# Kernel optimization log

Hardware: AMD Instinct MI355X
Metric: run time of the kernel (lower is better)

The kernel has to match this reference:

```python
import jax, jax.numpy as jnp
import numpy as np

B, N, E, H = 2, 4096, 768, 8
D = E // H
SCALING = float(D ** 0.5)


def setup_inputs() -> dict:
    key = jax.random.key(0)
    ks = jax.random.split(key, 9)
    s = 1.0 / np.sqrt(E)
    return {
        "x": jax.random.normal(ks[0], (B, N, E), dtype=jnp.float32),
        "Wq": jax.random.normal(ks[1], (E, E), dtype=jnp.float32) * s,
        "bq": jax.random.normal(ks[2], (E,), dtype=jnp.float32) * s,
        "Wk": jax.random.normal(ks[3], (E, E), dtype=jnp.float32) * s,
        "bk": jax.random.normal(ks[4], (E,), dtype=jnp.float32) * s,
        "Wv": jax.random.normal(ks[5], (E, E), dtype=jnp.float32) * s,
        "bv": jax.random.normal(ks[6], (E,), dtype=jnp.float32) * s,
        "Wo": jax.random.normal(ks[7], (E, E), dtype=jnp.float32) * s,
        "bo": jax.random.normal(ks[8], (E,), dtype=jnp.float32) * s,
    }


def reference(x, Wq, bq, Wk, bk, Wv, bv, Wo, bo):
    b, n, e = x.shape
    # projections, split heads: [b, n, e] -> [b, h, n, d]
    def split_heads(y):
        return y.reshape(b, n, H, D).transpose(0, 2, 1, 3)
    q = split_heads(x @ Wq + bq)
    k = split_heads(x @ Wk + bk)
    v = split_heads(x @ Wv + bv)
    # full quadratic attention matrix, as in the original einsum
    energy = jnp.einsum("bhqd,bhkd->bhqk", q, k)  # [b, h, n, n]
    # NOTE: original divides by scaling AFTER softmax (not before)
    att = jax.nn.softmax(energy, axis=-1) / SCALING
    out = jnp.einsum("bhqk,bhkd->bhqd", att, v)  # [b, h, n, d]
    out = out.transpose(0, 2, 1, 3).reshape(b, n, e)  # merge heads
    return out @ Wo + bo
```

## Files before the change

### kernel.cpp

```cpp
#include <hip/hip_runtime.h>
#include <hip/hip_bf16.h>


typedef unsigned short u16;
typedef unsigned long long u64;
typedef __attribute__((ext_vector_type(4))) float f32x4;
typedef __attribute__((ext_vector_type(8))) _Float16 h16x8;
typedef __attribute__((ext_vector_type(2))) __fp16 fp16x2;
typedef __attribute__((ext_vector_type(8))) u16 u16x8;

#define DEVI static __device__ __forceinline__

#define GLD16(gp, lp)                                                          \
  __builtin_amdgcn_global_load_lds(                                            \
      (const __attribute__((address_space(1))) void*)(gp),                     \
      (__attribute__((address_space(3))) void*)(lp), 16, 0, 0)
#define VM_WAIT6() asm volatile("s_waitcnt vmcnt(6)" ::: "memory")
#define VM_WAIT4() asm volatile("s_waitcnt vmcnt(4)" ::: "memory")
#define VM_WAIT0() asm volatile("s_waitcnt vmcnt(0)" ::: "memory")
#define BARRAW()   asm volatile("s_barrier" ::: "memory")

DEVI u16 f2h(float f) {
  _Float16 h = (_Float16)f;
  return __builtin_bit_cast(u16, h);
}

DEVI unsigned pkrtz(float a, float b) {
  fp16x2 h = __builtin_amdgcn_cvt_pkrtz(a, b);
  return __builtin_bit_cast(unsigned, h);
}

DEVI float exp2fast(float x) {
#if __has_builtin(__builtin_amdgcn_exp2f)
  return __builtin_amdgcn_exp2f(x);
#else
  return __expf(x * 0.6931471805599453f);
#endif
}

DEVI f32x4 mfma16(u16x8 a, u16x8 b, f32x4 c) {
  return __builtin_amdgcn_mfma_f32_16x16x32_f16(
      __builtin_bit_cast(h16x8, a), __builtin_bit_cast(h16x8, b), c, 0, 0, 0);
}

__global__ void k_cast(const float* __restrict__ x, u16* __restrict__ xh, int n8) {
  int i = blockIdx.x * blockDim.x + threadIdx.x;
  if (i >= n8) return;
  const f32x4* p = (const f32x4*)x + (size_t)i * 2;
  f32x4 a = p[0], b = p[1];
  u16x8 o;
  #pragma unroll
  for (int u = 0; u < 4; ++u) { o[u] = f2h(a[u]); o[4 + u] = f2h(b[u]); }
  *((u16x8*)xh + i) = o;
}

__global__ void k_wt(const float* __restrict__ Wq, const float* __restrict__ Wk,
                     const float* __restrict__ Wv, const float* __restrict__ Wo,
                     u16* __restrict__ wT) {
  __shared__ __align__(16) float T[64 * 68];
  int bid = blockIdx.x;
  int mat = bid / 144, tt = bid % 144;
  int tr = tt / 12, tc = tt % 12;
  const float* W = (mat == 0) ? Wq : (mat == 1) ? Wk : (mat == 2) ? Wv : Wo;
  int k0 = tr * 64, n0 = tc * 64;
  int t = threadIdx.x;
  #pragma unroll
  for (int ii = 0; ii < 4; ++ii) {
    int i = t + 256 * ii, r = i >> 4, c4 = i & 15;
    f32x4 v = *(const f32x4*)(W + (size_t)(k0 + r) * 768 + n0 + c4 * 4);
    *(f32x4*)(&T[r * 68 + c4 * 4]) = v;
  }
  __syncthreads();
  #pragma unroll
  for (int ii = 0; ii < 2; ++ii) {
    int i = t + 256 * ii, nn = i & 63, kc8 = i >> 6;
    u16x8 o;
    #pragma unroll
    for (int u = 0; u < 8; ++u) o[u] = f2h(T[(kc8 * 8 + u) * 68 + nn]);
    *(u16x8*)(wT + (size_t)mat * 589824 + (size_t)(n0 + nn) * 768 + k0 + kc8 * 8) = o;
  }
}

__global__ void k_vt(const u16* __restrict__ V, u16* __restrict__ Vt) {
  __shared__ __align__(16) u16 L[64 * 104];
  int bid = blockIdx.x, bh = bid >> 6, nb = bid & 63;
  int n0 = nb * 64, t = threadIdx.x;
  const u16* src = V + ((size_t)bh * 4096 + n0) * 96;
  #pragma unroll
  for (int ii = 0; ii < 3; ++ii) {
    int i = t + 256 * ii, r = i / 12, c8 = i % 12;
    *(u16x8*)(&L[r * 104 + c8 * 8]) = *(const u16x8*)(src + (size_t)i * 8);
  }
  __syncthreads();
  #pragma unroll
  for (int jj = 0; jj < 3; ++jj) {
    int d = (t & 31) + 32 * jj, c8 = t >> 5;
    u16x8 o;
    #pragma unroll
    for (int u = 0; u < 8; ++u) o[u] = L[(c8 * 8 + u) * 104 + d];
    *(u16x8*)(Vt + ((size_t)bh * 96 + d) * 4096 + n0 + c8 * 8) = o;
  }
}

template <int MODE>
__global__ __launch_bounds__(256) void k_gemm(
    const u16* __restrict__ A, const u16* __restrict__ BT,
    const float* __restrict__ bias0, const float* __restrict__ bias1,
    const float* __restrict__ bias2,
    u16* __restrict__ Qb, u16* __restrict__ Kb, u16* __restrict__ Vb,
    float* __restrict__ Out) {
  __shared__ __align__(16) u16 sg[16384];
  const int m0 = blockIdx.x * 128, n0 = blockIdx.y * 128;
  const int t = threadIdx.x, w = t >> 6, lane = t & 63;
  const int g = lane >> 4, c = lane & 15;
  const int wr = w >> 1, wc = w & 1;

  const u16* ap[2]; const u16* bp[2]; int lo[2];
  #pragma unroll
  for (int ii = 0; ii < 2; ++ii) {
    int i = t + 256 * ii;
    ap[ii] = A + (size_t)(m0 + (i >> 2)) * 768 + (i & 3) * 8;
    bp[ii] = BT + (size_t)(n0 + (i >> 2)) * 768 + (i & 3) * 8;
    lo[ii] = (i & ~63) * 8;
  }
  auto STAGE = [&](int buf) {
    #pragma unroll
    for (int ii = 0; ii < 2; ++ii) {
      GLD16(ap[ii], &sg[buf * 4096 + lo[ii]]);
      GLD16(bp[ii], &sg[8192 + buf * 4096 + lo[ii]]);
      ap[ii] += 32; bp[ii] += 32;
    }
  };

  f32x4 acc[4][4] = {};
  STAGE(0);
  #pragma unroll 1
  for (int kk = 0; kk < 24; ++kk) {
    const int cur = kk & 1;
    if (kk < 23) { STAGE(cur ^ 1); VM_WAIT4(); } else { VM_WAIT0(); }
    BARRAW();
    u16x8 af[4], bf[4];
    #pragma unroll
    for (int mt = 0; mt < 4; ++mt)
      af[mt] = *(u16x8*)(&sg[cur * 4096 + (wr * 64 + mt * 16 + c) * 32 + g * 8]);
    #pragma unroll
    for (int nt = 0; nt < 4; ++nt)
      bf[nt] = *(u16x8*)(&sg[8192 + cur * 4096 + (wc * 64 + nt * 16 + c) * 32 + g * 8]);
    #pragma unroll
    for (int mt = 0; mt < 4; ++mt)
      #pragma unroll
      for (int nt = 0; nt < 4; ++nt)
        acc[mt][nt] = mfma16(af[mt], bf[nt], acc[mt][nt]);
    BARRAW();
  }

  if (MODE == 0) {
    const int mat = n0 / 768;
    const float* bias = (mat == 0) ? bias0 : (mat == 1) ? bias1 : bias2;
    u16* dst = (mat == 0) ? Qb : (mat == 1) ? Kb : Vb;
    const float qsc = (mat == 0) ? 1.44269504f : 1.0f;
    const int nbase = n0 - mat * 768;
    #pragma unroll
    for (int mt = 0; mt < 4; ++mt)
      #pragma unroll
      for (int nt = 0; nt < 4; ++nt) {
        int ncol = nbase + wc * 64 + nt * 16 + c;
        int h = ncol / 96, d = ncol % 96;
        float bi = bias[ncol];
        #pragma unroll
        for (int r = 0; r < 4; ++r) {
          int mrow = m0 + wr * 64 + mt * 16 + g * 4 + r;
          int b = mrow >> 12, ntok = mrow & 4095;
          dst[((size_t)((b * 8 + h) * 4096 + ntok)) * 96 + d] =
              f2h((acc[mt][nt][r] + bi) * qsc);
        }
      }
  } else {
    #pragma unroll
    for (int mt = 0; mt < 4; ++mt)
      #pragma unroll
      for (int nt = 0; nt < 4; ++nt) {
        int ncol = n0 + wc * 64 + nt * 16 + c;
        float bi = bias0[ncol];
        #pragma unroll
        for (int r = 0; r < 4; ++r) {
          int mrow = m0 + wr * 64 + mt * 16 + g * 4 + r;
          Out[(size_t)mrow * 768 + ncol] = acc[mt][nt][r] + bi;
        }
      }
  }
}

__global__ __launch_bounds__(256) void k_attn(
    const u16* __restrict__ Q, const u16* __restrict__ K,
    const u16* __restrict__ Vt, u16* __restrict__ attn) {
  __shared__ __align__(16) u16 smem[34816];

  const int bid = blockIdx.x;
  const int bh = bid >> 5, qb = bid & 31;
  const int t = threadIdx.x, w = t >> 6, lane = t & 63;
  const int g = lane >> 4, c = lane & 15;
  const int q0 = qb * 128;

  u16x8 qf[3][2];
  #pragma unroll
  for (int qc = 0; qc < 2; ++qc) {
    const size_t qoff = ((size_t)bh * 4096 + q0 + w * 32 + qc * 16 + c) * 96;
    #pragma unroll
    for (int kc = 0; kc < 3; ++kc)
      qf[kc][qc] = *(const u16x8*)(Q + qoff + kc * 32 + g * 8);
  }
  VM_WAIT0();

  const u16* Kbb = K + (size_t)bh * 4096 * 96;
  const u16* Vtb = Vt + (size_t)bh * 96 * 4096;
  const u16* ks[3]; const u16* vs[3]; int ko[3], vo[3];
  #pragma unroll
  for (int ii = 0; ii < 3; ++ii) {
    int ci = t + 256 * ii;
    ks[ii] = Kbb + ci * 8;
    int d = ci >> 3, c8 = ci & 7;
    vs[ii] = Vtb + (size_t)d * 4096 + ((c8 ^ (d & 7)) * 8);
    ko[ii] = (ci & ~63) * 8;
    vo[ii] = 12288 + (ci & ~63) * 8;
  }
  auto STAGE = [&](int buf) {
    #pragma unroll
    for (int ii = 0; ii < 3; ++ii) {
      GLD16(ks[ii], &smem[buf * 6144 + ko[ii]]);
      GLD16(vs[ii], &smem[buf * 6144 + vo[ii]]);
      ks[ii] += 6144;
      vs[ii] += 64;
    }
  };

  f32x4 acc_o[6][2] = {};
  float m[2] = {-1e30f, -1e30f}, s[2] = {0.f, 0.f};
  u16* Pw = &smem[24576 + w * 2560];

  STAGE(0);
  #pragma unroll 1
  for (int tt = 0; tt < 64; ++tt) {
    const int cur = tt & 1;
    if (tt < 63) { STAGE(cur ^ 1); VM_WAIT6(); } else { VM_WAIT0(); }
    BARRAW();
    const u16* Kl = &smem[cur * 6144];
    const u16* Vl = &smem[12288 + cur * 6144];

    f32x4 et[4][2] = {};
    #pragma unroll
    for (int kc = 0; kc < 3; ++kc)
      #pragma unroll
      for (int mt = 0; mt < 4; ++mt) {
        u16x8 kf = *(const u16x8*)(&Kl[(mt * 16 + c) * 96 + kc * 32 + g * 8]);
        et[mt][0] = mfma16(kf, qf[kc][0], et[mt][0]);
        et[mt][1] = mfma16(kf, qf[kc][1], et[mt][1]);
      }

    #pragma unroll
    for (int qc = 0; qc < 2; ++qc) {
      float t0 = fmaxf(fmaxf(et[0][qc][0], et[0][qc][1]),
                       fmaxf(et[0][qc][2], et[0][qc][3]));
      float t1 = fmaxf(fmaxf(et[1][qc][0], et[1][qc][1]),
                       fmaxf(et[1][qc][2], et[1][qc][3]));
      float t2 = fmaxf(fmaxf(et[2][qc][0], et[2][qc][1]),
                       fmaxf(et[2][qc][2], et[2][qc][3]));
      float t3 = fmaxf(fmaxf(et[3][qc][0], et[3][qc][1]),
                       fmaxf(et[3][qc][2], et[3][qc][3]));
      float tmax = fmaxf(fmaxf(t0, t1), fmaxf(t2, t3));
      tmax = fmaxf(tmax, __shfl_xor(tmax, 16));
      tmax = fmaxf(tmax, __shfl_xor(tmax, 32));
      bool upd = tmax > m[qc] + 12.0f;
      float mnew = upd ? tmax : m[qc];
      if (__any(upd)) {
        float sc = exp2fast(m[qc] - mnew);
        s[qc] *= sc;
        #pragma unroll
        for (int dt = 0; dt < 6; ++dt)
          #pragma unroll
          for (int r = 0; r < 4; ++r) acc_o[dt][qc][r] *= sc;
      }
      m[qc] = mnew;
      float psum = 0.f;
      #pragma unroll
      for (int mt = 0; mt < 4; ++mt)
        #pragma unroll
        for (int r = 0; r < 4; ++r) {
          float p = exp2fast(et[mt][qc][r] - mnew);
          et[mt][qc][r] = p; psum += p;
        }
      psum += __shfl_xor(psum, 16);
      psum += __shfl_xor(psum, 32);
      s[qc] += psum;

      u16* P = Pw + qc * 1280;
      #pragma unroll
      for (int mt = 0; mt < 4; ++mt) {
        unsigned p0 = pkrtz(et[mt][qc][0], et[mt][qc][1]);
        unsigned p1 = pkrtz(et[mt][qc][2], et[mt][qc][3]);
        *(u64*)(&P[c * 80 + mt * 16 + g * 4]) = (u64)p0 | ((u64)p1 << 32);
      }
    }
    u16x8 pf[2][2];
    #pragma unroll
    for (int qc = 0; qc < 2; ++qc)
      #pragma unroll
      for (int kb = 0; kb < 2; ++kb)
        pf[qc][kb] = *(u16x8*)(&Pw[qc * 1280 + c * 80 + kb * 32 + g * 8]);
    #pragma unroll
    for (int dt = 0; dt < 6; ++dt)
      #pragma unroll
      for (int kb = 0; kb < 2; ++kb) {
        u16x8 vf = *(u16x8*)(&Vl[(dt * 16 + c) * 64 + (((kb * 4 + g) ^ (c & 7)) * 8)]);
        acc_o[dt][0] = mfma16(vf, pf[0][kb], acc_o[dt][0]);
        acc_o[dt][1] = mfma16(vf, pf[1][kb], acc_o[dt][1]);
      }
    BARRAW();
  }

  __syncthreads();
  u16* O = smem;
  #pragma unroll
  for (int qc = 0; qc < 2; ++qc) {
    const float inv = 1.0f / (s[qc] * 9.797958971132712f);
    #pragma unroll
    for (int dt = 0; dt < 6; ++dt)
      #pragma unroll
      for (int rp = 0; rp < 2; ++rp) {
        unsigned pk = (unsigned)f2h(acc_o[dt][qc][2 * rp] * inv) |
                      ((unsigned)f2h(acc_o[dt][qc][2 * rp + 1] * inv) << 16);
        *(unsigned*)(&O[(w * 32 + qc * 16 + c) * 96 + dt * 16 + g * 4 + 2 * rp]) = pk;
      }
  }
  __syncthreads();
  const int b = bh >> 3, h = bh & 7;
  #pragma unroll
  for (int ii = 0; ii < 6; ++ii) {
    int i = t + 256 * ii, r = i / 12, c8 = i % 12;
    u16x8 v = *(u16x8*)(&O[r * 96 + c8 * 8]);
    *(u16x8*)(attn + ((size_t)(b * 4096 + q0 + r)) * 768 + h * 96 + c8 * 8) = v;
  }
}

extern "C" void kernel_launch(void* const* d_in, const int* in_sizes, int n_in,
                              void* d_out, int out_size, void* d_ws, size_t ws_size,
                              hipStream_t stream) {
  const float* x  = (const float*)d_in[0];
  const float* Wq = (const float*)d_in[1];
  const float* bq = (const float*)d_in[2];
  const float* Wk = (const float*)d_in[3];
  const float* bk = (const float*)d_in[4];
  const float* Wv = (const float*)d_in[5];
  const float* bv = (const float*)d_in[6];
  const float* Wo = (const float*)d_in[7];
  const float* bo = (const float*)d_in[8];
  float* out = (float*)d_out;

  char* ws = (char*)d_ws;
  size_t off = 0;
  auto alloc = [&](size_t bytes) {
    void* p = ws + off;
    off += (bytes + 1023) & ~(size_t)1023;
    return p;
  };
  const size_t SZ = (size_t)16 * 4096 * 96 * 2;
  u16* xh    = (u16*)alloc((size_t)8192 * 768 * 2);
  u16* wT    = (u16*)alloc((size_t)4 * 768 * 768 * 2);
  u16* Qb    = (u16*)alloc(SZ);
  u16* Kb    = (u16*)alloc(SZ);
  u16* Vb    = (u16*)alloc(SZ);
  u16* Vtb   = (u16*)alloc(SZ);
  u16* attnb = (u16*)alloc(SZ);
  (void)ws_size; (void)in_sizes; (void)n_in; (void)out_size;

  k_cast<<<3072, 256, 0, stream>>>(x, xh, 786432);
  k_wt<<<576, 256, 0, stream>>>(Wq, Wk, Wv, Wo, wT);
  k_gemm<0><<<dim3(64, 18), 256, 0, stream>>>(xh, wT, bq, bk, bv,
                                              Qb, Kb, Vb, nullptr);
  k_vt<<<1024, 256, 0, stream>>>(Vb, Vtb);
  k_attn<<<512, 256, 0, stream>>>(Qb, Kb, Vtb, attnb);
  k_gemm<1><<<dim3(64, 6), 256, 0, stream>>>(attnb, wT + (size_t)3 * 589824,
                                             bo, nullptr, nullptr,
                                             nullptr, nullptr, nullptr, out);
}
```

Before: 314.3 us.

## Software-pipeline attention loop: defer PV MFMA by one tile, split K/V staging

Restructures the flash-attention inner loop so the P·V MFMAs for the previous key tile run after the current tile's QK^T MFMAs, overlapping softmax with matrix work. K and V loads are now staged separately: K for the next tile and V for the current tile are issued after a single barrier, which removes one barrier per iteration. The deferred rescale of the output accumulator is carried across iterations in scp/flp. The wait drops to vmcnt(0) each iteration, which may expose load latency that the old double-buffered prefetch hid.

```diff
diff --git a/kernel.cpp b/kernel.cpp
--- a/kernel.cpp
+++ b/kernel.cpp
@@ -15,7 +15,6 @@
   __builtin_amdgcn_global_load_lds(                                            \
       (const __attribute__((address_space(1))) void*)(gp),                     \
       (__attribute__((address_space(3))) void*)(lp), 16, 0, 0)
-#define VM_WAIT6() asm volatile("s_waitcnt vmcnt(6)" ::: "memory")
 #define VM_WAIT4() asm volatile("s_waitcnt vmcnt(4)" ::: "memory")
 #define VM_WAIT0() asm volatile("s_waitcnt vmcnt(0)" ::: "memory")
 #define BARRAW()   asm volatile("s_barrier" ::: "memory")
@@ -214,7 +213,7 @@
 
   const u16* Kbb = K + (size_t)bh * 4096 * 96;
   const u16* Vtb = Vt + (size_t)bh * 96 * 4096;
-  const u16* ks[3]; const u16* vs[3]; int ko[3], vo[3];
+  const u16* ks[3]; const u16* vs[3]; int ko[3];
   #pragma unroll
   for (int ii = 0; ii < 3; ++ii) {
     int ci = t + 256 * ii;
@@ -222,31 +221,39 @@
     int d = ci >> 3, c8 = ci & 7;
     vs[ii] = Vtb + (size_t)d * 4096 + ((c8 ^ (d & 7)) * 8);
     ko[ii] = (ci & ~63) * 8;
-    vo[ii] = 12288 + (ci & ~63) * 8;
-  }
-  auto STAGE = [&](int buf) {
+  }
+  auto STAGE_K = [&](int buf) {
     #pragma unroll
     for (int ii = 0; ii < 3; ++ii) {
       GLD16(ks[ii], &smem[buf * 6144 + ko[ii]]);
-      GLD16(vs[ii], &smem[buf * 6144 + vo[ii]]);
       ks[ii] += 6144;
+    }
+  };
+  auto STAGE_V = [&](int buf) {
+    #pragma unroll
+    for (int ii = 0; ii < 3; ++ii) {
+      GLD16(vs[ii], &smem[12288 + buf * 6144 + ko[ii]]);
       vs[ii] += 64;
     }
   };
 
   f32x4 acc_o[6][2] = {};
   float m[2] = {-1e30f, -1e30f}, s[2] = {0.f, 0.f};
+  float scp[2] = {1.f, 1.f};
+  bool flp[2] = {false, false};
+  u16x8 pf[2][2];
   u16* Pw = &smem[24576 + w * 2560];
 
-  STAGE(0);
+  STAGE_K(0);
   #pragma unroll 1
   for (int tt = 0; tt < 64; ++tt) {
     const int cur = tt & 1;
-    if (tt < 63) { STAGE(cur ^ 1); VM_WAIT6(); } else { VM_WAIT0(); }
+    VM_WAIT0();
     BARRAW();
+    if (tt < 63) STAGE_K(cur ^ 1);
+    STAGE_V(cur);
+
     const u16* Kl = &smem[cur * 6144];
-    const u16* Vl = &smem[12288 + cur * 6144];
-
     f32x4 et[4][2] = {};
     #pragma unroll
     for (int kc = 0; kc < 3; ++kc)
@@ -256,6 +263,27 @@
         et[mt][0] = mfma16(kf, qf[kc][0], et[mt][0]);
         et[mt][1] = mfma16(kf, qf[kc][1], et[mt][1]);
       }
+
+    if (tt > 0) {
+      const u16* Vp = &smem[12288 + (cur ^ 1) * 6144];
+      #pragma unroll
+      for (int qc = 0; qc < 2; ++qc)
+        if (flp[qc]) {
+          #pragma unroll
+          for (int dt = 0; dt < 6; ++dt)
+            #pragma unroll
+            for (int r = 0; r < 4; ++r) acc_o[dt][qc][r] *= scp[qc];
+        }
+      #pragma unroll
+      for (int dt = 0; dt < 6; ++dt)
+        #pragma unroll
+        for (int kb = 0; kb < 2; ++kb) {
+          u16x8 vf = *(const u16x8*)(&Vp[(dt * 16 + c) * 64 +
+                                         (((kb * 4 + g) ^ (c & 7)) * 8)]);
+          acc_o[dt][0] = mfma16(vf, pf[0][kb], acc_o[dt][0]);
+          acc_o[dt][1] = mfma16(vf, pf[1][kb], acc_o[dt][1]);
+        }
+    }
 
     #pragma unroll
     for (int qc = 0; qc < 2; ++qc) {
@@ -272,14 +300,7 @@
       tmax = fmaxf(tmax, __shfl_xor(tmax, 32));
       bool upd = tmax > m[qc] + 12.0f;
       float mnew = upd ? tmax : m[qc];
-      if (__any(upd)) {
-        float sc = exp2fast(m[qc] - mnew);
-        s[qc] *= sc;
-        #pragma unroll
-        for (int dt = 0; dt < 6; ++dt)
-          #pragma unroll
-          for (int r = 0; r < 4; ++r) acc_o[dt][qc][r] *= sc;
-      }
+      float sct = exp2fast(m[qc] - mnew);
       m[qc] = mnew;
       float psum = 0.f;
       #pragma unroll
@@ -291,7 +312,9 @@
         }
       psum += __shfl_xor(psum, 16);
       psum += __shfl_xor(psum, 32);
-      s[qc] += psum;
+      s[qc] = s[qc] * sct + psum;
+      scp[qc] = sct;
+      flp[qc] = __any(upd);
 
       u16* P = Pw + qc * 1280;
       #pragma unroll
@@ -301,21 +324,34 @@
         *(u64*)(&P[c * 80 + mt * 16 + g * 4]) = (u64)p0 | ((u64)p1 << 32);
       }
     }
-    u16x8 pf[2][2];
     #pragma unroll
     for (int qc = 0; qc < 2; ++qc)
       #pragma unroll
       for (int kb = 0; kb < 2; ++kb)
         pf[qc][kb] = *(u16x8*)(&Pw[qc * 1280 + c * 80 + kb * 32 + g * 8]);
+  }
+
+  VM_WAIT0();
+  BARRAW();
+  {
+    const u16* Vp = &smem[12288 + 1 * 6144];
+    #pragma unroll
+    for (int qc = 0; qc < 2; ++qc)
+      if (flp[qc]) {
+        #pragma unroll
+        for (int dt = 0; dt < 6; ++dt)
+          #pragma unroll
+          for (int r = 0; r < 4; ++r) acc_o[dt][qc][r] *= scp[qc];
+      }
     #pragma unroll
     for (int dt = 0; dt < 6; ++dt)
       #pragma unroll
       for (int kb = 0; kb < 2; ++kb) {
-        u16x8 vf = *(u16x8*)(&Vl[(dt * 16 + c) * 64 + (((kb * 4 + g) ^ (c & 7)) * 8)]);
+        u16x8 vf = *(const u16x8*)(&Vp[(dt * 16 + c) * 64 +
+                                       (((kb * 4 + g) ^ (c & 7)) * 8)]);
         acc_o[dt][0] = mfma16(vf, pf[0][kb], acc_o[dt][0]);
         acc_o[dt][1] = mfma16(vf, pf[1][kb], acc_o[dt][1]);
       }
-    BARRAW();
   }
 
   __syncthreads();
```

Result: no change. 317.1 us (+0.9%).
